# Optimization experiments

Measured on AMD Instinct MI355X. Metric: run time of the kernel, lower is better.

Reference implementation:

```python
import jax, jax.numpy as jnp
import numpy as np

WET_MIX = 0.3
FEEDBACK = 0.4
ROOM_SIZE = 0.5
NUM_REFL = 8
NUM_HEADS = 4

# Delay kernel table: int(delay) in {0,1,2,>=3} -> kernel_size {identity,3,5,7}.
# A k-tap kernel with padding k//2 == the same kernel zero-padded to 7 taps with padding 3.
def _gauss7(ks):
    g = np.exp(-np.linspace(-2.0, 2.0, ks) ** 2)
    g = g / g.sum()
    out = np.zeros(7, np.float32)
    s = (7 - ks) // 2
    out[s:s + ks] = g
    return out
_delta = np.zeros(7, np.float32); _delta[3] = 1.0
K_TABLE = jnp.asarray(np.stack([_delta, _gauss7(3), _gauss7(5), _gauss7(7)]))  # [4,7]


def _conv2d(x, w, b, pad):
    y = jax.lax.conv_general_dilated(x, w, (1, 1), [(pad, pad), (pad, pad)],
                                     dimension_numbers=('NCHW', 'OIHW', 'NCHW'))
    return y + b[None, :, None, None]


def _delay_line(x, kern7):
    # vertical depthwise Gaussian blur, same for every (batch, channel) plane
    b, c, h, w = x.shape
    k = kern7.reshape(1, 1, 7, 1)
    y = jax.lax.conv_general_dilated(x.reshape(b * c, 1, h, w), k, (1, 1), [(3, 3), (0, 0)],
                                     dimension_numbers=('NCHW', 'OIHW', 'NCHW'))
    return y.reshape(b, c, h, w)


def _forward(x, refl_w, refl_d, sc_w, sc_b, fb_w, fb_b, d1_w, d1_b, d2_w, d2_b,
             in_proj_w, in_proj_b, out_proj_w, out_proj_b, oc_w, oc_b):
    B, C, H, W = x.shape
    scaled = refl_d * ROOM_SIZE
    kidx = jnp.clip(jnp.floor(scaled).astype(jnp.int32), 0, 3)  # int(delay) detaches grad, as in torch

    wet = jnp.zeros_like(x)
    fb_buf = x * 0.1
    spatial = _conv2d(x, sc_w, sc_b, 1)  # [B,2C,H,W]

    for i in range(NUM_REFL):
        refl = _delay_line(fb_buf, K_TABLE[kidx[i]])
        refl = _conv2d(refl, fb_w, fb_b, 1)
        damp = jax.nn.sigmoid(_conv2d(jax.nn.silu(_conv2d(refl, d1_w, d1_b, 0)), d2_w, d2_b, 0))
        refl = refl * damp
        weight = jax.nn.sigmoid(refl_w[i]) * (0.8 ** i)
        wet = wet + refl * weight
        fb_buf = fb_buf + refl * (FEEDBACK * 0.1)

    # MultiheadAttention over L = H*W tokens, embed_dim=C=4, 4 heads (head_dim=1)
    L = H * W
    hd = C // NUM_HEADS
    wet_flat = wet.reshape(B, C, L).transpose(0, 2, 1)           # [B,L,C]
    qkv = wet_flat @ in_proj_w.T + in_proj_b                     # [B,L,3C]
    q, k, v = jnp.split(qkv, 3, axis=-1)
    def heads(t):
        return t.reshape(B, L, NUM_HEADS, hd).transpose(0, 2, 1, 3)  # [B,H,L,hd]
    q, k, v = heads(q), heads(k), heads(v)
    scores = jnp.einsum('bhqd,bhkd->bhqk', q, k) / np.sqrt(hd).astype(np.float32)
    attn = jax.nn.softmax(scores, axis=-1)
    o = jnp.einsum('bhqk,bhkd->bhqd', attn, v)
    o = o.transpose(0, 2, 1, 3).reshape(B, L, C) @ out_proj_w.T + out_proj_b
    wet2 = o.transpose(0, 2, 1).reshape(B, C, H, W)

    combined = jnp.concatenate([spatial, wet2], axis=1)          # [B,3C,H,W]
    processed_wet = _conv2d(combined, oc_w, oc_b, 0)
    return x * (1.0 - WET_MIX) + processed_wet * WET_MIX


def setup_inputs() -> dict:
    key = jax.random.key(0)
    ks = jax.random.split(key, 16)
    B, C, H, W = 2, 4, 64, 64
    f32 = jnp.float32
    return {
        'x': jax.random.normal(ks[0], (B, C, H, W), f32),
        'refl_w': jax.random.normal(ks[1], (8,), f32) * 0.1,
        'refl_d': jax.random.randint(ks[2], (8,), 1, 16).astype(f32),
        'sc_w': jax.random.normal(ks[3], (2 * C, C, 3, 3), f32) * 0.1,
        'sc_b': jnp.zeros((2 * C,), f32),
        'fb_w': jax.random.normal(ks[4], (C, C, 3, 3), f32) * 0.1,
        'fb_b': jnp.zeros((C,), f32),
        'd1_w': jax.random.normal(ks[5], (C // 2, C, 1, 1), f32) * 0.3,
        'd1_b': jnp.zeros((C // 2,), f32),
        'd2_w': jax.random.normal(ks[6], (C, C // 2, 1, 1), f32) * 0.3,
        'd2_b': jnp.zeros((C,), f32),
        'in_proj_w': jax.random.normal(ks[7], (3 * C, C), f32) * 0.3,
        'in_proj_b': jnp.zeros((3 * C,), f32),
        'out_proj_w': jax.random.normal(ks[8], (C, C), f32) * 0.3,
        'out_proj_b': jnp.zeros((C,), f32),
        'oc_w': jax.random.normal(ks[9], (C, 3 * C, 1, 1), f32) * 0.2,
        'oc_b': jnp.zeros((C,), f32),
    }


def reference(x, refl_w, refl_d, sc_w, sc_b, fb_w, fb_b, d1_w, d1_b, d2_w, d2_b,
              in_proj_w, in_proj_b, out_proj_w, out_proj_b, oc_w, oc_b):
    return _forward(x, refl_w, refl_d, sc_w, sc_b, fb_w, fb_b, d1_w, d1_b, d2_w, d2_b,
                    in_proj_w, in_proj_b, out_proj_w, out_proj_b, oc_w, oc_b)
```

## Files before the change

### kernel.cpp

```cpp
#include <hip/hip_runtime.h>
#include <math.h>


#define ZERO4 make_float4(0.f, 0.f, 0.f, 0.f)

__device__ __forceinline__ float sigf(float v) { return 1.0f / (1.0f + __expf(-v)); }

__device__ __forceinline__ float dppL(float v) {
    return __int_as_float(__builtin_amdgcn_mov_dpp(__float_as_int(v), 0x138, 0xf, 0xf, true));
}
__device__ __forceinline__ float dppR(float v) {
    return __int_as_float(__builtin_amdgcn_mov_dpp(__float_as_int(v), 0x130, 0xf, 0xf, true));
}
__device__ __forceinline__ float4 shL4(float4 v) {
    return make_float4(dppL(v.x), dppL(v.y), dppL(v.z), dppL(v.w));
}
__device__ __forceinline__ float4 shR4(float4 v) {
    return make_float4(dppR(v.x), dppR(v.y), dppR(v.z), dppR(v.w));
}

__device__ __forceinline__ void tap(float4& a, const float4 t, const float* wp) {
    a.x += wp[0]   * t.x + wp[9]    * t.y + wp[18]    * t.z + wp[27]    * t.w;
    a.y += wp[36]  * t.x + wp[36+9] * t.y + wp[36+18] * t.z + wp[36+27] * t.w;
    a.z += wp[72]  * t.x + wp[72+9] * t.y + wp[72+18] * t.z + wp[72+27] * t.w;
    a.w += wp[108] * t.x + wp[108+9]* t.y + wp[108+18]* t.z + wp[108+27]* t.w;
}

__global__ __launch_bounds__(1024, 1) void reverb_qkv_kernel(
    const float* __restrict__ x,
    const float* __restrict__ refl_w,
    const float* __restrict__ refl_d,
    const float* __restrict__ fb_w,
    const float* __restrict__ fb_b,
    const float* __restrict__ d1_w,
    const float* __restrict__ d1_b,
    const float* __restrict__ d2_w,
    const float* __restrict__ d2_b,
    const float* __restrict__ ipw,
    const float* __restrict__ ipb,
    float* __restrict__ Qg, float* __restrict__ Kg, float* __restrict__ Vg)
{
    __shared__ float4 P [18 * 64];
    __shared__ float4 BL[18 * 64];
    __shared__ float4 WT[2 * 64];
    __shared__ float  GT[3][8];

    const int blk   = blockIdx.x;
    const int batch = blk >> 5;
    const int own0  = (blk & 31) << 1;
    const int LB    = own0 - 8;
    const int tid   = threadIdx.x;
    const int wy    = tid >> 6;
    const int r     = tid & 63;

    if (tid < 3) {
        const int rr = tid + 1;
        const int ks = 2 * rr + 1;
        const int s  = (7 - ks) >> 1;
        const double step = 4.0 / (double)(ks - 1);
        double g[7]; double sum = 0.0;
        for (int t = 0; t < 7; ++t) {
            if (t < ks) { double u = -2.0 + step * (double)t; g[t] = exp(-u * u); sum += g[t]; }
        }
        for (int t = 0; t < 7; ++t) GT[tid][t] = 0.0f;
        for (int t = 0; t < ks; ++t) GT[tid][s + t] = (float)(g[t] / sum);
    }

    for (int idx = tid; idx < 18 * 64; idx += 1024) {
        const int lc  = idx >> 6;
        const int row = idx & 63;
        const int gc  = LB + lc;
        float4 v = ZERO4;
        if (gc >= 0 && gc < 64) {
            const int base = batch * 16384 + row * 64 + gc;
            v.x = 0.1f * x[base];
            v.y = 0.1f * x[base + 4096];
            v.z = 0.1f * x[base + 8192];
            v.w = 0.1f * x[base + 12288];
        }
        P[idx] = v;
    }
    __syncthreads();

    double w8 = 1.0;
    for (int j = 0; j < 8; ++j) {
        int kidx = (int)floorf(refl_d[j] * 0.5f);
        kidx = kidx < 0 ? 0 : (kidx > 3 ? 3 : kidx);
        float kv[7];
        #pragma unroll
        for (int u = 0; u < 7; ++u) {
            const float dv = (u == 3) ? 1.0f : 0.0f;
            kv[u] = (kidx == 0) ? dv : GT[kidx - 1][u];
        }
        const float wgt = sigf(refl_w[j]) * (float)w8;

        const int clo = max(0, own0 - (7 - j));
        const int chi = min(64, own0 + 2 + (7 - j));

        const int lcA   = (clo - 1) - LB;
        const int nBlur = (chi + 1) - (clo - 1);
        for (int t = wy; t < nBlur; t += 16) {
            const int lc = lcA + t;
            const int gc = LB + lc;
            float4 b = ZERO4;
            if (gc >= 0 && gc < 64) {
                const float4 v  = P[lc * 64 + r];
                const float4 l1 = shL4(v),  l2 = shL4(l1), l3 = shL4(l2);
                const float4 r1 = shR4(v),  r2 = shR4(r1), r3 = shR4(r2);
                b.x = kv[0]*l3.x + kv[1]*l2.x + kv[2]*l1.x + kv[3]*v.x
                    + kv[4]*r1.x + kv[5]*r2.x + kv[6]*r3.x;
                b.y = kv[0]*l3.y + kv[1]*l2.y + kv[2]*l1.y + kv[3]*v.y
                    + kv[4]*r1.y + kv[5]*r2.y + kv[6]*r3.y;
                b.z = kv[0]*l3.z + kv[1]*l2.z + kv[2]*l1.z + kv[3]*v.z
                    + kv[4]*r1.z + kv[5]*r2.z + kv[6]*r3.z;
                b.w = kv[0]*l3.w + kv[1]*l2.w + kv[2]*l1.w + kv[3]*v.w
                    + kv[4]*r1.w + kv[5]*r2.w + kv[6]*r3.w;
            }
            BL[lc * 64 + r] = b;
        }
        __syncthreads();

        const int c = clo + wy;
        if (wy < chi - clo) {
            const int lc = c - LB;
            const float4 bm = BL[(lc - 1) * 64 + r];
            const float4 bc = BL[lc * 64 + r];
            const float4 bp = BL[(lc + 1) * 64 + r];

            float4 acc = make_float4(fb_b[0], fb_b[1], fb_b[2], fb_b[3]);
            tap(acc, shL4(bm), fb_w + 0);  tap(acc, shL4(bc), fb_w + 1);  tap(acc, shL4(bp), fb_w + 2);
            tap(acc, bm,       fb_w + 3);  tap(acc, bc,       fb_w + 4);  tap(acc, bp,       fb_w + 5);
            tap(acc, shR4(bm), fb_w + 6);  tap(acc, shR4(bc), fb_w + 7);  tap(acc, shR4(bp), fb_w + 8);

            float4 rr = acc;
            float h0 = d1_b[0] + d1_w[0]*rr.x + d1_w[1]*rr.y + d1_w[2]*rr.z + d1_w[3]*rr.w;
            float h1 = d1_b[1] + d1_w[4]*rr.x + d1_w[5]*rr.y + d1_w[6]*rr.z + d1_w[7]*rr.w;
            h0 = h0 * sigf(h0);
            h1 = h1 * sigf(h1);
            const float d0  = sigf(d2_b[0] + d2_w[0]*h0 + d2_w[1]*h1);
            const float d1v = sigf(d2_b[1] + d2_w[2]*h0 + d2_w[3]*h1);
            const float d2v = sigf(d2_b[2] + d2_w[4]*h0 + d2_w[5]*h1);
            const float d3v = sigf(d2_b[3] + d2_w[6]*h0 + d2_w[7]*h1);
            rr.x *= d0; rr.y *= d1v; rr.z *= d2v; rr.w *= d3v;

            const float4 oldfb = P[lc * 64 + r];
            P[lc * 64 + r] = make_float4(oldfb.x + 0.04f*rr.x, oldfb.y + 0.04f*rr.y,
                                         oldfb.z + 0.04f*rr.z, oldfb.w + 0.04f*rr.w);

            if (c >= own0 && c < own0 + 2) {
                const int widx = (c - own0) * 64 + r;
                float4 wv = make_float4(wgt*rr.x, wgt*rr.y, wgt*rr.z, wgt*rr.w);
                if (j > 0) {
                    const float4 old = WT[widx];
                    wv.x += old.x; wv.y += old.y; wv.z += old.z; wv.w += old.w;
                }
                WT[widx] = wv;
            }
        }
        __syncthreads();
        w8 *= 0.8;
    }

    if (tid < 128) {
        const int row = tid & 63;
        const int oc  = tid >> 6;
        const int c   = own0 + oc;
        const float4 wv = WT[oc * 64 + row];
        #pragma unroll
        for (int h = 0; h < 4; ++h) {
            const float q = ipb[h]
                + ipw[h*4+0]*wv.x + ipw[h*4+1]*wv.y
                + ipw[h*4+2]*wv.z + ipw[h*4+3]*wv.w;
            const float k = ipb[4+h]
                + ipw[(4+h)*4+0]*wv.x + ipw[(4+h)*4+1]*wv.y
                + ipw[(4+h)*4+2]*wv.z + ipw[(4+h)*4+3]*wv.w;
            const float v = ipb[8+h]
                + ipw[(8+h)*4+0]*wv.x + ipw[(8+h)*4+1]*wv.y
                + ipw[(8+h)*4+2]*wv.z + ipw[(8+h)*4+3]*wv.w;
            const int o = (batch * 4 + h) * 4096 + row * 64 + c;
            Qg[o] = q; Kg[o] = k; Vg[o] = v;
        }
    }
}

__global__ __launch_bounds__(256) void attn_kernel(
    const float* __restrict__ Qg, const float* __restrict__ Kg,
    const float* __restrict__ Vg, float* __restrict__ OH)
{
    __shared__ float wred[8];
    __shared__ float partN[256], partD[256];

    const int bh  = blockIdx.x >> 6;
    const int sub = blockIdx.x & 63;
    const int tid = threadIdx.x;

    const float* Kp = Kg + bh * 4096;
    const float* Vp = Vg + bh * 4096;

    float pmax = -3.0e38f, pmin = 3.0e38f;
    for (int t = tid; t < 4096; t += 256) {
        const float kk = Kp[t];
        pmax = fmaxf(pmax, kk);
        pmin = fminf(pmin, kk);
    }
    #pragma unroll
    for (int off = 32; off > 0; off >>= 1) {
        pmax = fmaxf(pmax, __shfl_xor(pmax, off, 64));
        pmin = fminf(pmin, __shfl_xor(pmin, off, 64));
    }
    if ((tid & 63) == 0) { wred[tid >> 6] = pmax; wred[4 + (tid >> 6)] = pmin; }
    __syncthreads();
    const float kmax = fmaxf(fmaxf(wred[0], wred[1]), fmaxf(wred[2], wred[3]));
    const float kmin = fminf(fminf(wred[4], wred[5]), fminf(wred[6], wred[7]));

    const int ql = tid & 63;
    const int kh = __builtin_amdgcn_readfirstlane(tid >> 6);
    const int qi = sub * 64 + ql;

    const float L2E = 1.4426950408889634f;
    const float q  = Qg[bh * 4096 + qi];
    const float q2 = q * L2E;
    const float nm2 = -(((q >= 0.0f) ? q * kmax : q * kmin) * L2E);

    const float4* K4 = (const float4*)Kp;
    const float4* V4 = (const float4*)Vp;
    const int base = kh * 256;

    float num0 = 0.f, num1 = 0.f, den0 = 0.f, den1 = 0.f;
    #pragma unroll 4
    for (int j = 0; j < 256; j += 2) {
        const float4 ka = K4[base + j];
        const float4 kb = K4[base + j + 1];
        const float4 va = V4[base + j];
        const float4 vb = V4[base + j + 1];
        float e;
        e = __builtin_amdgcn_exp2f(__fmaf_rn(q2, ka.x, nm2)); den0 += e; num0 = __fmaf_rn(e, va.x, num0);
        e = __builtin_amdgcn_exp2f(__fmaf_rn(q2, ka.y, nm2)); den1 += e; num1 = __fmaf_rn(e, va.y, num1);
        e = __builtin_amdgcn_exp2f(__fmaf_rn(q2, ka.z, nm2)); den0 += e; num0 = __fmaf_rn(e, va.z, num0);
        e = __builtin_amdgcn_exp2f(__fmaf_rn(q2, ka.w, nm2)); den1 += e; num1 = __fmaf_rn(e, va.w, num1);
        e = __builtin_amdgcn_exp2f(__fmaf_rn(q2, kb.x, nm2)); den0 += e; num0 = __fmaf_rn(e, vb.x, num0);
        e = __builtin_amdgcn_exp2f(__fmaf_rn(q2, kb.y, nm2)); den1 += e; num1 = __fmaf_rn(e, vb.y, num1);
        e = __builtin_amdgcn_exp2f(__fmaf_rn(q2, kb.z, nm2)); den0 += e; num0 = __fmaf_rn(e, vb.z, num0);
        e = __builtin_amdgcn_exp2f(__fmaf_rn(q2, kb.w, nm2)); den1 += e; num1 = __fmaf_rn(e, vb.w, num1);
    }
    partN[tid] = num0 + num1;
    partD[tid] = den0 + den1;
    __syncthreads();
    if (tid < 64) {
        const float n = partN[tid] + partN[tid + 64] + partN[tid + 128] + partN[tid + 192];
        const float d = partD[tid] + partD[tid + 64] + partD[tid + 128] + partD[tid + 192];
        OH[bh * 4096 + sub * 64 + tid] = n / d;
    }
}

__global__ __launch_bounds__(128) void final_kernel(
    const float* __restrict__ x,
    const float* __restrict__ sc_w, const float* __restrict__ sc_b,
    const float* __restrict__ opw,  const float* __restrict__ opb,
    const float* __restrict__ ocw,  const float* __restrict__ ocb,
    const float* __restrict__ OH,   float* __restrict__ out)
{
    const int g   = blockIdx.x * 128 + threadIdx.x;
    const int b   = g >> 12;
    const int pix = g & 4095;
    const int y   = pix >> 6;
    const int xc  = pix & 63;

    float xin[4][3][3];
    #pragma unroll
    for (int ic = 0; ic < 4; ++ic)
        #pragma unroll
        for (int ky = 0; ky < 3; ++ky)
            #pragma unroll
            for (int kx = 0; kx < 3; ++kx) {
                const int yy = y + ky - 1, xx = xc + kx - 1;
                xin[ic][ky][kx] = (yy >= 0 && yy < 64 && xx >= 0 && xx < 64)
                                    ? x[(b * 4 + ic) * 4096 + yy * 64 + xx] : 0.f;
            }

    float sp[8];
    #pragma unroll
    for (int oc = 0; oc < 8; ++oc) {
        float a = sc_b[oc];
        #pragma unroll
        for (int ic = 0; ic < 4; ++ic)
            #pragma unroll
            for (int ky = 0; ky < 3; ++ky)
                #pragma unroll
                for (int kx = 0; kx < 3; ++kx)
                    a += sc_w[(oc * 4 + ic) * 9 + ky * 3 + kx] * xin[ic][ky][kx];
        sp[oc] = a;
    }

    float oh[4];
    #pragma unroll
    for (int h = 0; h < 4; ++h) oh[h] = OH[(b * 4 + h) * 4096 + pix];

    float w2[4];
    #pragma unroll
    for (int c = 0; c < 4; ++c)
        w2[c] = opb[c] + opw[c*4+0]*oh[0] + opw[c*4+1]*oh[1]
                       + opw[c*4+2]*oh[2] + opw[c*4+3]*oh[3];

    #pragma unroll
    for (int c = 0; c < 4; ++c) {
        float a = ocb[c];
        #pragma unroll
        for (int j = 0; j < 8; ++j) a += ocw[c * 12 + j] * sp[j];
        #pragma unroll
        for (int h = 0; h < 4; ++h) a += ocw[c * 12 + 8 + h] * w2[h];
        const int idx = (b * 4 + c) * 4096 + y * 64 + xc;
        out[idx] = 0.7f * x[idx] + 0.3f * a;
    }
}

extern "C" void kernel_launch(void* const* d_in, const int* in_sizes, int n_in,
                              void* d_out, int out_size, void* d_ws, size_t ws_size,
                              hipStream_t stream) {
    const float* x      = (const float*)d_in[0];
    const float* refl_w = (const float*)d_in[1];
    const float* refl_d = (const float*)d_in[2];
    const float* sc_w   = (const float*)d_in[3];
    const float* sc_b   = (const float*)d_in[4];
    const float* fb_w   = (const float*)d_in[5];
    const float* fb_b   = (const float*)d_in[6];
    const float* d1_w   = (const float*)d_in[7];
    const float* d1_b   = (const float*)d_in[8];
    const float* d2_w   = (const float*)d_in[9];
    const float* d2_b   = (const float*)d_in[10];
    const float* ipw    = (const float*)d_in[11];
    const float* ipb    = (const float*)d_in[12];
    const float* opw    = (const float*)d_in[13];
    const float* opb    = (const float*)d_in[14];
    const float* ocw    = (const float*)d_in[15];
    const float* ocb    = (const float*)d_in[16];
    float* out = (float*)d_out;

    float* Q  = (float*)d_ws;
    float* K  = Q + 32768;
    float* V  = K + 32768;
    float* OH = V + 32768;

    reverb_qkv_kernel<<<dim3(64), dim3(1024), 0, stream>>>(
        x, refl_w, refl_d, fb_w, fb_b, d1_w, d1_b, d2_w, d2_b, ipw, ipb,
        Q, K, V);
    attn_kernel<<<dim3(512), dim3(256), 0, stream>>>(Q, K, V, OH);
    final_kernel<<<dim3(64), dim3(128), 0, stream>>>(
        x, sc_w, sc_b, opw, opb, ocw, ocb, OH, out);
}
```

Baseline: 141.4 us.

## Split reverb work to one column per block and widen attention key split

The reverb kernel now gives each block a single output column with 256 threads across 128 blocks, where before each block handled two columns with 1024 threads across 64 blocks. Each block recomputes its own halo, so the redundant halo work roughly doubles, but more blocks run at once. The attention kernel now splits keys across 8 wavefronts instead of 4, which shortens each thread's serial loop at the cost of a larger reduction. Both changes aim to raise parallelism and latency hiding on a GPU that was underfilled.

```diff
diff --git a/kernel.cpp b/kernel.cpp
--- a/kernel.cpp
+++ b/kernel.cpp
@@ -26,7 +26,7 @@
     a.w += wp[108] * t.x + wp[108+9]* t.y + wp[108+18]* t.z + wp[108+27]* t.w;
 }
 
-__global__ __launch_bounds__(1024, 1) void reverb_qkv_kernel(
+__global__ __launch_bounds__(256) void reverb_qkv_kernel(
     const float* __restrict__ x,
     const float* __restrict__ refl_w,
     const float* __restrict__ refl_d,
@@ -40,15 +40,15 @@
     const float* __restrict__ ipb,
     float* __restrict__ Qg, float* __restrict__ Kg, float* __restrict__ Vg)
 {
-    __shared__ float4 P [18 * 64];
-    __shared__ float4 BL[18 * 64];
-    __shared__ float4 WT[2 * 64];
+    __shared__ float4 P [17 * 64];
+    __shared__ float4 BL[17 * 64];
+    __shared__ float4 WT[64];
     __shared__ float  GT[3][8];
 
     const int blk   = blockIdx.x;
-    const int batch = blk >> 5;
-    const int own0  = (blk & 31) << 1;
-    const int LB    = own0 - 8;
+    const int batch = blk >> 6;
+    const int c0    = blk & 63;
+    const int LB    = c0 - 8;
     const int tid   = threadIdx.x;
     const int wy    = tid >> 6;
     const int r     = tid & 63;
@@ -66,7 +66,7 @@
         for (int t = 0; t < ks; ++t) GT[tid][s + t] = (float)(g[t] / sum);
     }
 
-    for (int idx = tid; idx < 18 * 64; idx += 1024) {
+    for (int idx = tid; idx < 17 * 64; idx += 256) {
         const int lc  = idx >> 6;
         const int row = idx & 63;
         const int gc  = LB + lc;
@@ -94,12 +94,13 @@
         }
         const float wgt = sigf(refl_w[j]) * (float)w8;
 
-        const int clo = max(0, own0 - (7 - j));
-        const int chi = min(64, own0 + 2 + (7 - j));
+        const int rad = 7 - j;
+        const int clo = max(0, c0 - rad);
+        const int chi = min(64, c0 + rad + 1);
 
         const int lcA   = (clo - 1) - LB;
         const int nBlur = (chi + 1) - (clo - 1);
-        for (int t = wy; t < nBlur; t += 16) {
+        for (int t = wy; t < nBlur; t += 4) {
             const int lc = lcA + t;
             const int gc = LB + lc;
             float4 b = ZERO4;
@@ -120,8 +121,8 @@
         }
         __syncthreads();
 
-        const int c = clo + wy;
-        if (wy < chi - clo) {
+        for (int t = wy; t < chi - clo; t += 4) {
+            const int c  = clo + t;
             const int lc = c - LB;
             const float4 bm = BL[(lc - 1) * 64 + r];
             const float4 bc = BL[lc * 64 + r];
@@ -147,25 +148,21 @@
             P[lc * 64 + r] = make_float4(oldfb.x + 0.04f*rr.x, oldfb.y + 0.04f*rr.y,
                                          oldfb.z + 0.04f*rr.z, oldfb.w + 0.04f*rr.w);
 
-            if (c >= own0 && c < own0 + 2) {
-                const int widx = (c - own0) * 64 + r;
+            if (c == c0) {
                 float4 wv = make_float4(wgt*rr.x, wgt*rr.y, wgt*rr.z, wgt*rr.w);
                 if (j > 0) {
-                    const float4 old = WT[widx];
+                    const float4 old = WT[r];
                     wv.x += old.x; wv.y += old.y; wv.z += old.z; wv.w += old.w;
                 }
-                WT[widx] = wv;
+                WT[r] = wv;
             }
         }
         __syncthreads();
         w8 *= 0.8;
     }
 
-    if (tid < 128) {
-        const int row = tid & 63;
-        const int oc  = tid >> 6;
-        const int c   = own0 + oc;
-        const float4 wv = WT[oc * 64 + row];
+    if (tid < 64) {
+        const float4 wv = WT[tid];
         #pragma unroll
         for (int h = 0; h < 4; ++h) {
             const float q = ipb[h]
@@ -177,18 +174,18 @@
             const float v = ipb[8+h]
                 + ipw[(8+h)*4+0]*wv.x + ipw[(8+h)*4+1]*wv.y
                 + ipw[(8+h)*4+2]*wv.z + ipw[(8+h)*4+3]*wv.w;
-            const int o = (batch * 4 + h) * 4096 + row * 64 + c;
+            const int o = (batch * 4 + h) * 4096 + tid * 64 + c0;
             Qg[o] = q; Kg[o] = k; Vg[o] = v;
         }
     }
 }
 
-__global__ __launch_bounds__(256) void attn_kernel(
+__global__ __launch_bounds__(512) void attn_kernel(
     const float* __restrict__ Qg, const float* __restrict__ Kg,
     const float* __restrict__ Vg, float* __restrict__ OH)
 {
-    __shared__ float wred[8];
-    __shared__ float partN[256], partD[256];
+    __shared__ float wred[16];
+    __shared__ float partN[512], partD[512];
 
     const int bh  = blockIdx.x >> 6;
     const int sub = blockIdx.x & 63;
@@ -198,7 +195,7 @@
     const float* Vp = Vg + bh * 4096;
 
     float pmax = -3.0e38f, pmin = 3.0e38f;
-    for (int t = tid; t < 4096; t += 256) {
+    for (int t = tid; t < 4096; t += 512) {
         const float kk = Kp[t];
         pmax = fmaxf(pmax, kk);
         pmin = fminf(pmin, kk);
@@ -208,10 +205,14 @@
         pmax = fmaxf(pmax, __shfl_xor(pmax, off, 64));
         pmin = fminf(pmin, __shfl_xor(pmin, off, 64));
     }
-    if ((tid & 63) == 0) { wred[tid >> 6] = pmax; wred[4 + (tid >> 6)] = pmin; }
+    if ((tid & 63) == 0) { wred[tid >> 6] = pmax; wred[8 + (tid >> 6)] = pmin; }
     __syncthreads();
-    const float kmax = fmaxf(fmaxf(wred[0], wred[1]), fmaxf(wred[2], wred[3]));
-    const float kmin = fminf(fminf(wred[4], wred[5]), fminf(wred[6], wred[7]));
+    float kmax = wred[0], kmin = wred[8];
+    #pragma unroll
+    for (int w = 1; w < 8; ++w) {
+        kmax = fmaxf(kmax, wred[w]);
+        kmin = fminf(kmin, wred[8 + w]);
+    }
 
     const int ql = tid & 63;
     const int kh = __builtin_amdgcn_readfirstlane(tid >> 6);
@@ -224,11 +225,11 @@
 
     const float4* K4 = (const float4*)Kp;
     const float4* V4 = (const float4*)Vp;
-    const int base = kh * 256;
+    const int base = kh * 128;
 
     float num0 = 0.f, num1 = 0.f, den0 = 0.f, den1 = 0.f;
     #pragma unroll 4
-    for (int j = 0; j < 256; j += 2) {
+    for (int j = 0; j < 128; j += 2) {
         const float4 ka = K4[base + j];
         const float4 kb = K4[base + j + 1];
         const float4 va = V4[base + j];
@@ -247,8 +248,12 @@
     partD[tid] = den0 + den1;
     __syncthreads();
     if (tid < 64) {
-        const float n = partN[tid] + partN[tid + 64] + partN[tid + 128] + partN[tid + 192];
-        const float d = partD[tid] + partD[tid + 64] + partD[tid + 128] + partD[tid + 192];
+        float n = 0.f, d = 0.f;
+        #pragma unroll
+        for (int w = 0; w < 8; ++w) {
+            n += partN[tid + 64 * w];
+            d += partD[tid + 64 * w];
+        }
         OH[bh * 4096 + sub * 64 + tid] = n / d;
     }
 }
@@ -341,10 +346,10 @@
     float* V  = K + 32768;
     float* OH = V + 32768;
 
-    reverb_qkv_kernel<<<dim3(64), dim3(1024), 0, stream>>>(
+    reverb_qkv_kernel<<<dim3(128), dim3(256), 0, stream>>>(
         x, refl_w, refl_d, fb_w, fb_b, d1_w, d1_b, d2_w, d2_b, ipw, ipb,
         Q, K, V);
-    attn_kernel<<<dim3(512), dim3(256), 0, stream>>>(Q, K, V, OH);
+    attn_kernel<<<dim3(512), dim3(512), 0, stream>>>(Q, K, V, OH);
     final_kernel<<<dim3(64), dim3(128), 0, stream>>>(
         x, sc_w, sc_b, opw, opb, ocw, ocb, OH, out);
 }
```

New measurement: 161.4 us. 14.1% more time.

## Make reverb kernel one wavefront per column with register-resident state; split K min/max

Applied to the files above, without the earlier changes.

The reverb kernel now runs one 64-thread wavefront per output column instead of a 1024-thread block covering two columns. The 17-column halo of the feedback buffer and the blur results are held in registers, so LDS and block barriers are no longer needed. The cost is redundant halo recomputation per column and fewer resident threads overall. The per-head K max/min reduction moves out of every attention block into a separate small kernel, trading repeated reductions for an extra launch.

```diff
diff --git a/kernel.cpp b/kernel.cpp
--- a/kernel.cpp
+++ b/kernel.cpp
@@ -26,7 +26,22 @@
     a.w += wp[108] * t.x + wp[108+9]* t.y + wp[108+18]* t.z + wp[108+27]* t.w;
 }
 
-__global__ __launch_bounds__(1024, 1) void reverb_qkv_kernel(
+__device__ __forceinline__ float4 blurP(float4 v, const float* kv) {
+    const float4 l1 = shL4(v),  l2 = shL4(l1), l3 = shL4(l2);
+    const float4 r1 = shR4(v),  r2 = shR4(r1), r3 = shR4(r2);
+    float4 b;
+    b.x = kv[0]*l3.x + kv[1]*l2.x + kv[2]*l1.x + kv[3]*v.x
+        + kv[4]*r1.x + kv[5]*r2.x + kv[6]*r3.x;
+    b.y = kv[0]*l3.y + kv[1]*l2.y + kv[2]*l1.y + kv[3]*v.y
+        + kv[4]*r1.y + kv[5]*r2.y + kv[6]*r3.y;
+    b.z = kv[0]*l3.z + kv[1]*l2.z + kv[2]*l1.z + kv[3]*v.z
+        + kv[4]*r1.z + kv[5]*r2.z + kv[6]*r3.z;
+    b.w = kv[0]*l3.w + kv[1]*l2.w + kv[2]*l1.w + kv[3]*v.w
+        + kv[4]*r1.w + kv[5]*r2.w + kv[6]*r3.w;
+    return b;
+}
+
+__global__ __launch_bounds__(64, 1) void reverb_qkv_kernel(
     const float* __restrict__ x,
     const float* __restrict__ refl_w,
     const float* __restrict__ refl_d,
@@ -40,48 +55,46 @@
     const float* __restrict__ ipb,
     float* __restrict__ Qg, float* __restrict__ Kg, float* __restrict__ Vg)
 {
-    __shared__ float4 P [18 * 64];
-    __shared__ float4 BL[18 * 64];
-    __shared__ float4 WT[2 * 64];
-    __shared__ float  GT[3][8];
-
     const int blk   = blockIdx.x;
-    const int batch = blk >> 5;
-    const int own0  = (blk & 31) << 1;
-    const int LB    = own0 - 8;
-    const int tid   = threadIdx.x;
-    const int wy    = tid >> 6;
-    const int r     = tid & 63;
-
-    if (tid < 3) {
-        const int rr = tid + 1;
+    const int batch = blk >> 6;
+    const int c0    = blk & 63;
+    const int r     = threadIdx.x;
+
+    float gt[3][7];
+    #pragma unroll
+    for (int rr = 1; rr <= 3; ++rr) {
         const int ks = 2 * rr + 1;
         const int s  = (7 - ks) >> 1;
         const double step = 4.0 / (double)(ks - 1);
         double g[7]; double sum = 0.0;
+        #pragma unroll
         for (int t = 0; t < 7; ++t) {
             if (t < ks) { double u = -2.0 + step * (double)t; g[t] = exp(-u * u); sum += g[t]; }
-        }
-        for (int t = 0; t < 7; ++t) GT[tid][t] = 0.0f;
-        for (int t = 0; t < ks; ++t) GT[tid][s + t] = (float)(g[t] / sum);
-    }
-
-    for (int idx = tid; idx < 18 * 64; idx += 1024) {
-        const int lc  = idx >> 6;
-        const int row = idx & 63;
-        const int gc  = LB + lc;
+            else g[t] = 0.0;
+        }
+        #pragma unroll
+        for (int t = 0; t < 7; ++t) gt[rr - 1][t] = 0.0f;
+        #pragma unroll
+        for (int t = 0; t < 7; ++t)
+            if (t < ks) gt[rr - 1][s + t] = (float)(g[t] / sum);
+    }
+
+    float4 P[17];
+    #pragma unroll
+    for (int i = 0; i < 17; ++i) {
+        const int gc = c0 - 8 + i;
         float4 v = ZERO4;
         if (gc >= 0 && gc < 64) {
-            const int base = batch * 16384 + row * 64 + gc;
+            const int base = batch * 16384 + r * 64 + gc;
             v.x = 0.1f * x[base];
             v.y = 0.1f * x[base + 4096];
             v.z = 0.1f * x[base + 8192];
             v.w = 0.1f * x[base + 12288];
         }
-        P[idx] = v;
-    }
-    __syncthreads();
-
+        P[i] = v;
+    }
+
+    float4 wet = ZERO4;
     double w8 = 1.0;
     for (int j = 0; j < 8; ++j) {
         int kidx = (int)floorf(refl_d[j] * 0.5f);
@@ -90,82 +103,63 @@
         #pragma unroll
         for (int u = 0; u < 7; ++u) {
             const float dv = (u == 3) ? 1.0f : 0.0f;
-            kv[u] = (kidx == 0) ? dv : GT[kidx - 1][u];
+            kv[u] = (kidx == 0) ? dv
+                  : (kidx == 1) ? gt[0][u]
+                  : (kidx == 2) ? gt[1][u]
+                                : gt[2][u];
         }
         const float wgt = sigf(refl_w[j]) * (float)w8;
-
-        const int clo = max(0, own0 - (7 - j));
-        const int chi = min(64, own0 + 2 + (7 - j));
-
-        const int lcA   = (clo - 1) - LB;
-        const int nBlur = (chi + 1) - (clo - 1);
-        for (int t = wy; t < nBlur; t += 16) {
-            const int lc = lcA + t;
-            const int gc = LB + lc;
-            float4 b = ZERO4;
-            if (gc >= 0 && gc < 64) {
-                const float4 v  = P[lc * 64 + r];
-                const float4 l1 = shL4(v),  l2 = shL4(l1), l3 = shL4(l2);
-                const float4 r1 = shR4(v),  r2 = shR4(r1), r3 = shR4(r2);
-                b.x = kv[0]*l3.x + kv[1]*l2.x + kv[2]*l1.x + kv[3]*v.x
-                    + kv[4]*r1.x + kv[5]*r2.x + kv[6]*r3.x;
-                b.y = kv[0]*l3.y + kv[1]*l2.y + kv[2]*l1.y + kv[3]*v.y
-                    + kv[4]*r1.y + kv[5]*r2.y + kv[6]*r3.y;
-                b.z = kv[0]*l3.z + kv[1]*l2.z + kv[2]*l1.z + kv[3]*v.z
-                    + kv[4]*r1.z + kv[5]*r2.z + kv[6]*r3.z;
-                b.w = kv[0]*l3.w + kv[1]*l2.w + kv[2]*l1.w + kv[3]*v.w
-                    + kv[4]*r1.w + kv[5]*r2.w + kv[6]*r3.w;
+        const int rad = 7 - j;
+
+        float4 bm = ZERO4, bc = ZERO4;
+        #pragma unroll
+        for (int i = 0; i <= 16; ++i) {
+            float4 bnew = ZERO4;
+            if (i >= 7 - rad && i <= 9 + rad)
+                bnew = blurP(P[i], kv);
+
+            const int ic = i - 1;
+            if (ic >= 1 && ic >= 8 - rad && ic <= 8 + rad) {
+                const int c = c0 - 8 + ic;
+                if (c >= 0 && c < 64) {
+                    float4 acc = make_float4(fb_b[0], fb_b[1], fb_b[2], fb_b[3]);
+                    tap(acc, shL4(bm),   fb_w + 0);
+                    tap(acc, shL4(bc),   fb_w + 1);
+                    tap(acc, shL4(bnew), fb_w + 2);
+                    tap(acc, bm,         fb_w + 3);
+                    tap(acc, bc,         fb_w + 4);
+                    tap(acc, bnew,       fb_w + 5);
+                    tap(acc, shR4(bm),   fb_w + 6);
+                    tap(acc, shR4(bc),   fb_w + 7);
+                    tap(acc, shR4(bnew), fb_w + 8);
+
+                    float4 rr = acc;
+                    float h0 = d1_b[0] + d1_w[0]*rr.x + d1_w[1]*rr.y + d1_w[2]*rr.z + d1_w[3]*rr.w;
+                    float h1 = d1_b[1] + d1_w[4]*rr.x + d1_w[5]*rr.y + d1_w[6]*rr.z + d1_w[7]*rr.w;
+                    h0 = h0 * sigf(h0);
+                    h1 = h1 * sigf(h1);
+                    const float d0  = sigf(d2_b[0] + d2_w[0]*h0 + d2_w[1]*h1);
+                    const float d1v = sigf(d2_b[1] + d2_w[2]*h0 + d2_w[3]*h1);
+                    const float d2v = sigf(d2_b[2] + d2_w[4]*h0 + d2_w[5]*h1);
+                    const float d3v = sigf(d2_b[3] + d2_w[6]*h0 + d2_w[7]*h1);
+                    rr.x *= d0; rr.y *= d1v; rr.z *= d2v; rr.w *= d3v;
+
+                    P[ic] = make_float4(P[ic].x + 0.04f*rr.x, P[ic].y + 0.04f*rr.y,
+                                        P[ic].z + 0.04f*rr.z, P[ic].w + 0.04f*rr.w);
+
+                    if (ic == 8) {
+                        wet.x += wgt*rr.x;  wet.y += wgt*rr.y;
+                        wet.z += wgt*rr.z;  wet.w += wgt*rr.w;
+                    }
+                }
             }
-            BL[lc * 64 + r] = b;
-        }
-        __syncthreads();
-
-        const int c = clo + wy;
-        if (wy < chi - clo) {
-            const int lc = c - LB;
-            const float4 bm = BL[(lc - 1) * 64 + r];
-            const float4 bc = BL[lc * 64 + r];
-            const float4 bp = BL[(lc + 1) * 64 + r];
-
-            float4 acc = make_float4(fb_b[0], fb_b[1], fb_b[2], fb_b[3]);
-            tap(acc, shL4(bm), fb_w + 0);  tap(acc, shL4(bc), fb_w + 1);  tap(acc, shL4(bp), fb_w + 2);
-            tap(acc, bm,       fb_w + 3);  tap(acc, bc,       fb_w + 4);  tap(acc, bp,       fb_w + 5);
-            tap(acc, shR4(bm), fb_w + 6);  tap(acc, shR4(bc), fb_w + 7);  tap(acc, shR4(bp), fb_w + 8);
-
-            float4 rr = acc;
-            float h0 = d1_b[0] + d1_w[0]*rr.x + d1_w[1]*rr.y + d1_w[2]*rr.z + d1_w[3]*rr.w;
-            float h1 = d1_b[1] + d1_w[4]*rr.x + d1_w[5]*rr.y + d1_w[6]*rr.z + d1_w[7]*rr.w;
-            h0 = h0 * sigf(h0);
-            h1 = h1 * sigf(h1);
-            const float d0  = sigf(d2_b[0] + d2_w[0]*h0 + d2_w[1]*h1);
-            const float d1v = sigf(d2_b[1] + d2_w[2]*h0 + d2_w[3]*h1);
-            const float d2v = sigf(d2_b[2] + d2_w[4]*h0 + d2_w[5]*h1);
-            const float d3v = sigf(d2_b[3] + d2_w[6]*h0 + d2_w[7]*h1);
-            rr.x *= d0; rr.y *= d1v; rr.z *= d2v; rr.w *= d3v;
-
-            const float4 oldfb = P[lc * 64 + r];
-            P[lc * 64 + r] = make_float4(oldfb.x + 0.04f*rr.x, oldfb.y + 0.04f*rr.y,
-                                         oldfb.z + 0.04f*rr.z, oldfb.w + 0.04f*rr.w);
-
-            if (c >= own0 && c < own0 + 2) {
-                const int widx = (c - own0) * 64 + r;
-                float4 wv = make_float4(wgt*rr.x, wgt*rr.y, wgt*rr.z, wgt*rr.w);
-                if (j > 0) {
-                    const float4 old = WT[widx];
-                    wv.x += old.x; wv.y += old.y; wv.z += old.z; wv.w += old.w;
-                }
-                WT[widx] = wv;
-            }
-        }
-        __syncthreads();
+            bm = bc; bc = bnew;
+        }
         w8 *= 0.8;
     }
 
-    if (tid < 128) {
-        const int row = tid & 63;
-        const int oc  = tid >> 6;
-        const int c   = own0 + oc;
-        const float4 wv = WT[oc * 64 + row];
+    {
+        const float4 wv = wet;
         #pragma unroll
         for (int h = 0; h < 4; ++h) {
             const float q = ipb[h]
@@ -177,26 +171,19 @@
             const float v = ipb[8+h]
                 + ipw[(8+h)*4+0]*wv.x + ipw[(8+h)*4+1]*wv.y
                 + ipw[(8+h)*4+2]*wv.z + ipw[(8+h)*4+3]*wv.w;
-            const int o = (batch * 4 + h) * 4096 + row * 64 + c;
+            const int o = (batch * 4 + h) * 4096 + r * 64 + c0;
             Qg[o] = q; Kg[o] = k; Vg[o] = v;
         }
     }
 }
 
-__global__ __launch_bounds__(256) void attn_kernel(
-    const float* __restrict__ Qg, const float* __restrict__ Kg,
-    const float* __restrict__ Vg, float* __restrict__ OH)
+__global__ __launch_bounds__(256) void kminmax_kernel(
+    const float* __restrict__ Kg, float* __restrict__ KM)
 {
-    __shared__ float wred[8];
-    __shared__ float partN[256], partD[256];
-
-    const int bh  = blockIdx.x >> 6;
-    const int sub = blockIdx.x & 63;
+    __shared__ float red[8];
+    const int bh = blockIdx.x;
     const int tid = threadIdx.x;
-
     const float* Kp = Kg + bh * 4096;
-    const float* Vp = Vg + bh * 4096;
-
     float pmax = -3.0e38f, pmin = 3.0e38f;
     for (int t = tid; t < 4096; t += 256) {
         const float kk = Kp[t];
@@ -208,10 +195,30 @@
         pmax = fmaxf(pmax, __shfl_xor(pmax, off, 64));
         pmin = fminf(pmin, __shfl_xor(pmin, off, 64));
     }
-    if ((tid & 63) == 0) { wred[tid >> 6] = pmax; wred[4 + (tid >> 6)] = pmin; }
+    if ((tid & 63) == 0) { red[tid >> 6] = pmax; red[4 + (tid >> 6)] = pmin; }
     __syncthreads();
-    const float kmax = fmaxf(fmaxf(wred[0], wred[1]), fmaxf(wred[2], wred[3]));
-    const float kmin = fminf(fminf(wred[4], wred[5]), fminf(wred[6], wred[7]));
+    if (tid == 0) {
+        KM[bh]     = fmaxf(fmaxf(red[0], red[1]), fmaxf(red[2], red[3]));
+        KM[8 + bh] = fminf(fminf(red[4], red[5]), fminf(red[6], red[7]));
+    }
+}
+
+__global__ __launch_bounds__(256) void attn_kernel(
+    const float* __restrict__ Qg, const float* __restrict__ Kg,
+    const float* __restrict__ Vg, const float* __restrict__ KM,
+    float* __restrict__ OH)
+{
+    __shared__ float partN[256], partD[256];
+
+    const int bh  = blockIdx.x >> 6;
+    const int sub = blockIdx.x & 63;
+    const int tid = threadIdx.x;
+
+    const float* Kp = Kg + bh * 4096;
+    const float* Vp = Vg + bh * 4096;
+
+    const float kmax = KM[bh];
+    const float kmin = KM[8 + bh];
 
     const int ql = tid & 63;
     const int kh = __builtin_amdgcn_readfirstlane(tid >> 6);
@@ -340,11 +347,13 @@
     float* K  = Q + 32768;
     float* V  = K + 32768;
     float* OH = V + 32768;
-
-    reverb_qkv_kernel<<<dim3(64), dim3(1024), 0, stream>>>(
+    float* KM = OH + 32768;
+
+    reverb_qkv_kernel<<<dim3(128), dim3(64), 0, stream>>>(
         x, refl_w, refl_d, fb_w, fb_b, d1_w, d1_b, d2_w, d2_b, ipw, ipb,
         Q, K, V);
-    attn_kernel<<<dim3(512), dim3(256), 0, stream>>>(Q, K, V, OH);
+    kminmax_kernel<<<dim3(8), dim3(256), 0, stream>>>(K, KM);
+    attn_kernel<<<dim3(512), dim3(256), 0, stream>>>(Q, K, V, KM, OH);
     final_kernel<<<dim3(64), dim3(128), 0, stream>>>(
         x, sc_w, sc_b, opw, opb, ocw, ocb, OH, out);
 }
```

Measured after the change: 193.1 us. 36.6% more time.

## Split attention key dimension across four blocks with partial sums reduced in final kernel

Applied to the files above, without the earlier changes.

The attention kernel now splits the 4096-key range into four chunks, each handled by a separate block, which raises the grid from 512 to 2048 blocks. Each block writes partial numerator and denominator sums to workspace, and the final kernel adds the four partials before dividing. The aim is more parallelism and better occupancy across the GPU's compute units. The cost is that every block recomputes the full K min/max reduction, and the extra partial buffers add workspace traffic.

```diff
diff --git a/kernel.cpp b/kernel.cpp
--- a/kernel.cpp
+++ b/kernel.cpp
@@ -185,13 +185,15 @@
 
 __global__ __launch_bounds__(256) void attn_kernel(
     const float* __restrict__ Qg, const float* __restrict__ Kg,
-    const float* __restrict__ Vg, float* __restrict__ OH)
+    const float* __restrict__ Vg,
+    float* __restrict__ PN, float* __restrict__ PD)
 {
     __shared__ float wred[8];
     __shared__ float partN[256], partD[256];
 
-    const int bh  = blockIdx.x >> 6;
-    const int sub = blockIdx.x & 63;
+    const int bh  = blockIdx.x >> 8;
+    const int sub = (blockIdx.x >> 2) & 63;
+    const int ks  = blockIdx.x & 3;
     const int tid = threadIdx.x;
 
     const float* Kp = Kg + bh * 4096;
@@ -224,11 +226,11 @@
 
     const float4* K4 = (const float4*)Kp;
     const float4* V4 = (const float4*)Vp;
-    const int base = kh * 256;
+    const int base = ks * 256 + kh * 64;
 
     float num0 = 0.f, num1 = 0.f, den0 = 0.f, den1 = 0.f;
     #pragma unroll 4
-    for (int j = 0; j < 256; j += 2) {
+    for (int j = 0; j < 64; j += 2) {
         const float4 ka = K4[base + j];
         const float4 kb = K4[base + j + 1];
         const float4 va = V4[base + j];
@@ -249,7 +251,9 @@
     if (tid < 64) {
         const float n = partN[tid] + partN[tid + 64] + partN[tid + 128] + partN[tid + 192];
         const float d = partD[tid] + partD[tid + 64] + partD[tid + 128] + partD[tid + 192];
-        OH[bh * 4096 + sub * 64 + tid] = n / d;
+        const int o = bh * 16384 + ks * 4096 + sub * 64 + tid;
+        PN[o] = n;
+        PD[o] = d;
     }
 }
 
@@ -258,7 +262,8 @@
     const float* __restrict__ sc_w, const float* __restrict__ sc_b,
     const float* __restrict__ opw,  const float* __restrict__ opb,
     const float* __restrict__ ocw,  const float* __restrict__ ocb,
-    const float* __restrict__ OH,   float* __restrict__ out)
+    const float* __restrict__ PN,   const float* __restrict__ PD,
+    float* __restrict__ out)
 {
     const int g   = blockIdx.x * 128 + threadIdx.x;
     const int b   = g >> 12;
@@ -294,7 +299,16 @@
 
     float oh[4];
     #pragma unroll
-    for (int h = 0; h < 4; ++h) oh[h] = OH[(b * 4 + h) * 4096 + pix];
+    for (int h = 0; h < 4; ++h) {
+        const int bh = b * 4 + h;
+        float n = 0.f, d = 0.f;
+        #pragma unroll
+        for (int ks = 0; ks < 4; ++ks) {
+            n += PN[bh * 16384 + ks * 4096 + pix];
+            d += PD[bh * 16384 + ks * 4096 + pix];
+        }
+        oh[h] = n / d;
+    }
 
     float w2[4];
     #pragma unroll
@@ -339,12 +353,13 @@
     float* Q  = (float*)d_ws;
     float* K  = Q + 32768;
     float* V  = K + 32768;
-    float* OH = V + 32768;
+    float* PN = V + 32768;
+    float* PD = PN + 131072;
 
     reverb_qkv_kernel<<<dim3(64), dim3(1024), 0, stream>>>(
         x, refl_w, refl_d, fb_w, fb_b, d1_w, d1_b, d2_w, d2_b, ipw, ipb,
         Q, K, V);
-    attn_kernel<<<dim3(512), dim3(256), 0, stream>>>(Q, K, V, OH);
+    attn_kernel<<<dim3(2048), dim3(256), 0, stream>>>(Q, K, V, PN, PD);
     final_kernel<<<dim3(64), dim3(128), 0, stream>>>(
-        x, sc_w, sc_b, opw, opb, ocw, ocb, OH, out);
-}
+        x, sc_w, sc_b, opw, opb, ocw, ocb, PN, PD, out);
+}
```

Result: no change. 139.5 us (-1.4%).
